# Optimization experiments

Measured on AMD Instinct MI355X. Metric: run time of the kernel, lower is better.

## Reference

```python
import jax, jax.numpy as jnp
import numpy as np

# Regularized layout for the per-batch masked attention:
#   batch_size B=8, each batch has NF=2048 'fill' points followed by NK=4096 'keep' points.
B, NF, NK = 8, 2048, 4096
C_IN, C_KQ, C_OUT = 256, 64, 256


def setup_inputs() -> dict:
    key = jax.random.key(0)
    ks = jax.random.split(key, 7)
    N = B * (NF + NK)
    features = jax.random.normal(ks[0], (N, C_IN), dtype=jnp.float32)
    # keep flag: 0 for fill points, 1 for keep points, per batch (fill-first layout)
    flag = jnp.tile(jnp.concatenate([jnp.zeros(NF, jnp.int32), jnp.ones(NK, jnp.int32)]), B)
    s = 1.0 / np.sqrt(C_IN)
    Wq = jax.random.normal(ks[1], (C_KQ, C_IN), jnp.float32) * s
    bq = jnp.zeros((C_KQ,), jnp.float32)
    Wk = jax.random.normal(ks[2], (C_KQ, C_IN), jnp.float32) * s
    bk = jnp.zeros((C_KQ,), jnp.float32)
    Wv = jax.random.normal(ks[3], (C_OUT, C_IN), jnp.float32) * s
    bv = jnp.zeros((C_OUT,), jnp.float32)
    return {"features": features, "keep_flag": flag,
            "Wq": Wq, "bq": bq, "Wk": Wk, "bk": bk, "Wv": Wv, "bv": bv}


def reference(features, keep_flag, Wq, bq, Wk, bk, Wv, bv):
    # features: [N, C_IN]; keep_flag encodes the fill/keep split, which in this
    # regular layout is: first NF rows of each batch are fill, remaining NK are keep.
    del keep_flag  # structure is encoded in the layout (fill-first per batch)
    f = features.reshape(B, NF + NK, C_IN)
    fill = f[:, :NF]             # [B, NF, C_IN]
    keep = f[:, NF:]             # [B, NK, C_IN]
    q = fill @ Wq.T + bq         # [B, NF, C_KQ]
    k = keep @ Wk.T + bk         # [B, NK, C_KQ]
    v = keep @ Wv.T + bv         # [B, NK, C_OUT]
    ratio = np.sqrt(C_KQ).astype(np.float32)
    scores = jnp.einsum('bfd,bkd->bfk', q, k) / ratio   # [B, NF, NK]
    attn = jax.nn.softmax(scores, axis=-1)
    out_fill = jnp.einsum('bfk,bkc->bfc', attn, v)      # [B, NF, C_OUT]
    # keep rows pass through unchanged (only fill rows are overwritten)
    out = jnp.concatenate([out_fill, keep], axis=1)
    return out.reshape(B * (NF + NK), C_OUT)
```

## Files before the change

kernel.cpp:

```cpp
#include <hip/hip_runtime.h>
#include <hip/hip_bf16.h>

#define BATCHES 8
#define NFILL 2048
#define NKEEP 4096
#define SEQLEN 6144
#define CIN 256
#define CKQ 64
#define COUT 256

#define KSC 0.18033688011112042f
#define KOFF -11.541560327111707f

typedef __bf16 bf16_t;
typedef float f32x4 __attribute__((ext_vector_type(4)));
typedef bf16_t bf16x8 __attribute__((ext_vector_type(8)));

__device__ inline void cvt8_store(bf16_t* dst, float4 a, float4 b) {
  bf16x8 v;
  v[0] = (bf16_t)a.x; v[1] = (bf16_t)a.y; v[2] = (bf16_t)a.z; v[3] = (bf16_t)a.w;
  v[4] = (bf16_t)b.x; v[5] = (bf16_t)b.y; v[6] = (bf16_t)b.z; v[7] = (bf16_t)b.w;
  *(bf16x8*)dst = v;
}

__device__ inline void proj_tile(const bf16_t (*Xs)[264], bf16_t (*Ws)[72],
                                 const float* __restrict__ Wmat, int lr,
                                 int koff, int wv, int l16, int quad,
                                 f32x4 acc[4]) {
  const float* wp = Wmat + (long)lr * CIN + koff;
  float4 w0 = *(const float4*)(wp);
  float4 w1 = *(const float4*)(wp + 4);
  float4 w2 = *(const float4*)(wp + 8);
  float4 w3 = *(const float4*)(wp + 12);
#pragma unroll
  for (int nb = 0; nb < 4; nb++) acc[nb] = f32x4{0.f, 0.f, 0.f, 0.f};
#pragma unroll
  for (int k0 = 0; k0 < CIN; k0 += 64) {
    const int kn = (k0 + 64 < CIN) ? k0 + 64 : k0;
    float4 n0 = *(const float4*)(wp + kn);
    float4 n1 = *(const float4*)(wp + kn + 4);
    float4 n2 = *(const float4*)(wp + kn + 8);
    float4 n3 = *(const float4*)(wp + kn + 12);
    __syncthreads();
    cvt8_store(&Ws[lr][koff], w0, w1);
    cvt8_store(&Ws[lr][koff + 8], w2, w3);
    __syncthreads();
#pragma unroll
    for (int ks = 0; ks < 2; ks++) {
      bf16x8 afrag = *(const bf16x8*)&Xs[wv * 16 + l16][k0 + ks * 32 + quad * 8];
#pragma unroll
      for (int nb = 0; nb < 4; nb++) {
        bf16x8 bfrag = *(const bf16x8*)&Ws[nb * 16 + l16][ks * 32 + quad * 8];
        acc[nb] = __builtin_amdgcn_mfma_f32_16x16x32_bf16(afrag, bfrag, acc[nb], 0, 0, 0);
      }
    }
    w0 = n0; w1 = n1; w2 = n2; w3 = n3;
  }
}

__global__ __launch_bounds__(256) void gemm_qkv(
    const float* __restrict__ feat, const float* __restrict__ Wq,
    const float* __restrict__ bq, const float* __restrict__ Wk,
    const float* __restrict__ bk, const float* __restrict__ Wv,
    const float* __restrict__ bv, bf16_t* __restrict__ Qw,
    bf16_t* __restrict__ Kw, bf16_t* __restrict__ Vw,
    float* __restrict__ outp) {
  __shared__ bf16_t Xs[64][264];
  __shared__ bf16_t Ws[64][72];
  __shared__ float Cs[64][68];

  const int bid = blockIdx.x;
  const bool isQ = bid >= 512;
  const int mb = isQ ? bid - 512 : bid;

  const int t = threadIdx.x;
  const int lane = t & 63;
  const int wv = t >> 6;
  const int l16 = lane & 15;
  const int quad = lane >> 4;

  const int lr = t >> 2;
  const int koff = (t & 3) << 4;

  const int mrow = mb * 64 + lr;
  const int rpb_shift = isQ ? 11 : 12;
  const int batch = mrow >> rpb_shift;
  const int ridx = mrow & ((1 << rpb_shift) - 1);
  const int row_off = isQ ? 0 : NFILL;
  const long grow = (long)(batch * SEQLEN + row_off + ridx);
  const float* xptr = feat + grow * CIN;
  float4* orow = (float4*)(outp + grow * COUT);

#pragma unroll
  for (int j = 0; j < 4; j++) {
    const int c = koff + j * 64;
    float4 x0 = *(const float4*)(xptr + c);
    float4 x1 = *(const float4*)(xptr + c + 4);
    float4 x2 = *(const float4*)(xptr + c + 8);
    float4 x3 = *(const float4*)(xptr + c + 12);
    cvt8_store(&Xs[lr][c], x0, x1);
    cvt8_store(&Xs[lr][c + 8], x2, x3);
    if (!isQ) {
      orow[(c >> 2) + 0] = x0;
      orow[(c >> 2) + 1] = x1;
      orow[(c >> 2) + 2] = x2;
      orow[(c >> 2) + 3] = x3;
    }
  }
  __syncthreads();

  f32x4 acc[4];

  if (isQ) {
    proj_tile(Xs, Ws, Wq, lr, koff, wv, l16, quad, acc);
#pragma unroll
    for (int nb = 0; nb < 4; nb++) {
      const int n = nb * 16 + l16;
      const float bb = bq[n];
#pragma unroll
      for (int r = 0; r < 4; r++) {
        const int m = mb * 64 + wv * 16 + quad * 4 + r;
        Qw[(long)m * CKQ + n] = (bf16_t)(acc[nb][r] + bb);
      }
    }
    return;
  }

  proj_tile(Xs, Ws, Wk, lr, koff, wv, l16, quad, acc);
#pragma unroll
  for (int nb = 0; nb < 4; nb++) {
    const int n = nb * 16 + l16;
    const float bb = bk[n];
#pragma unroll
    for (int r = 0; r < 4; r++) {
      const int m = mb * 64 + wv * 16 + quad * 4 + r;
      Kw[(long)m * CKQ + n] = (bf16_t)(acc[nb][r] + bb);
    }
  }

  const int vb = (mb * 64) >> 12;
  const int key0base = (mb * 64) & 4095;
  for (int nt = 0; nt < 4; nt++) {
    const int n0 = nt * 64;
    proj_tile(Xs, Ws, Wv + (long)n0 * CIN, lr, koff, wv, l16, quad, acc);

    __syncthreads();
#pragma unroll
    for (int nb = 0; nb < 4; nb++) {
      const float bb = bv[n0 + nb * 16 + l16];
#pragma unroll
      for (int r = 0; r < 4; r++)
        Cs[wv * 16 + quad * 4 + r][nb * 16 + l16] = acc[nb][r] + bb;
    }
    __syncthreads();
    const int c = t >> 2;
    const int seg = t & 3;
    bf16_t tmp[16];
#pragma unroll
    for (int i = 0; i < 16; i++) tmp[i] = (bf16_t)Cs[seg * 16 + i][c];
    bf16_t* dst = Vw + ((long)(vb * COUT + n0 + c)) * NKEEP + key0base + seg * 16;
    *(uint4*)dst = *(uint4*)tmp;
    *(uint4*)(dst + 8) = *(uint4*)(tmp + 8);
  }
}

__global__ __launch_bounds__(256) void attn_kernel(
    const bf16_t* __restrict__ Q, const bf16_t* __restrict__ K,
    const bf16_t* __restrict__ Vt, float* __restrict__ outp) {
  __shared__ bf16_t Ks[2][64][72];
  __shared__ bf16_t Ps[64][72];
  __shared__ float Lsh[64];

  const int qt = blockIdx.x;
  const int b = blockIdx.y;
  const int t = threadIdx.x;
  const int lane = t & 63;
  const int wv = t >> 6;
  const int l16 = lane & 15;
  const int quad = lane >> 4;

  const int krow = t >> 2;
  const int kcol = (t & 3) << 4;

  const bf16_t* kbase = K + (long)b * NKEEP * CKQ;
  const int c0 = wv * 64;
  const bf16_t* vlane =
      Vt + ((long)(b * COUT + c0 + l16)) * NKEEP + quad * 8;

  bf16x8 qfrag[2];
  {
    const bf16_t* qrow = Q + ((long)(b * NFILL + qt * 64 + wv * 16 + l16)) * CKQ;
#pragma unroll
    for (int ks = 0; ks < 2; ks++)
      qfrag[ks] = *(const bf16x8*)(qrow + ks * 32 + quad * 8);
  }

  f32x4 oacc[4][4];
#pragma unroll
  for (int m = 0; m < 4; m++)
#pragma unroll
    for (int ct = 0; ct < 4; ct++) oacc[m][ct] = f32x4{0.f, 0.f, 0.f, 0.f};
  float rsum[4] = {0.f, 0.f, 0.f, 0.f};

  uint4 kreg0, kreg1;
  bf16x8 vA[8], vB[8];

  {
    const bf16_t* ksrc = kbase + (long)krow * CKQ + kcol;
    uint4 k0 = *(const uint4*)ksrc;
    uint4 k1 = *(const uint4*)(ksrc + 8);
#pragma unroll
    for (int ct = 0; ct < 4; ct++)
#pragma unroll
      for (int ks = 0; ks < 2; ks++)
        vA[ct * 2 + ks] = *(const bf16x8*)(vlane + (long)ct * 16 * NKEEP + ks * 32);
    *(uint4*)&Ks[0][krow][kcol] = k0;
    *(uint4*)&Ks[0][krow][kcol + 8] = k1;
  }

#define ATTN_TILE(BUF, VCUR, VNEXT, TV)                                         \
  {                                                                             \
    __syncthreads(); \
    const int tn = ((TV) + 1 < 64) ? (TV) + 1 : 63;                             \
    {                                                                           \
      const bf16_t* ksrc = kbase + ((long)(tn * 64 + krow)) * CKQ + kcol;       \
      kreg0 = *(const uint4*)ksrc;                                              \
      kreg1 = *(const uint4*)(ksrc + 8);                                        \
      const bf16_t* vsrc = vlane + (long)tn * 64;                               \
      _Pragma("unroll") for (int ct = 0; ct < 4; ct++)                          \
          _Pragma("unroll") for (int ks = 0; ks < 2; ks++)                      \
              VNEXT[ct * 2 + ks] =                                              \
          *(const bf16x8*)(vsrc + (long)ct * 16 * NKEEP + ks * 32);             \
    }                                                                           \
    f32x4 sacc[4];                                                              \
    _Pragma("unroll") for (int nb = 0; nb < 4; nb++)                            \
        sacc[nb] = f32x4{0.f, 0.f, 0.f, 0.f};                                   \
    _Pragma("unroll") for (int ks = 0; ks < 2; ks++) {                          \
      _Pragma("unroll") for (int nb = 0; nb < 4; nb++) {                        \
        bf16x8 kfrag = *(const bf16x8*)&Ks[BUF][nb * 16 + l16][ks * 32 + quad * 8]; \
        sacc[nb] = __builtin_amdgcn_mfma_f32_16x16x32_bf16(qfrag[ks], kfrag,    \
                                                           sacc[nb], 0, 0, 0); \
      }                                                                         \
    }                                                                           \
    _Pragma("unroll") for (int nb = 0; nb < 4; nb++) {                          \
      _Pragma("unroll") for (int r = 0; r < 4; r++) {                           \
        const float p = __builtin_exp2f(fmaf(sacc[nb][r], KSC, KOFF));          \
        rsum[r] += p;                                                           \
        Ps[wv * 16 + quad * 4 + r][nb * 16 + l16] = (bf16_t)p;                  \
      }                                                                         \
    }                                                                           \
    asm volatile("s_waitcnt lgkmcnt(0)\n\ts_barrier" ::: "memory");      \
    _Pragma("unroll") for (int ks = 0; ks < 2; ks++) {                          \
      _Pragma("unroll") for (int m = 0; m < 4; m++) {                           \
        bf16x8 pfrag = *(const bf16x8*)&Ps[m * 16 + l16][ks * 32 + quad * 8];   \
        _Pragma("unroll") for (int ct = 0; ct < 4; ct++)                        \
            oacc[m][ct] = __builtin_amdgcn_mfma_f32_16x16x32_bf16(              \
                pfrag, VCUR[ct * 2 + ks], oacc[m][ct], 0, 0, 0);                \
      }                                                                         \
    }                                                                           \
    *(uint4*)&Ks[BUF ^ 1][krow][kcol] = kreg0;                                  \
    *(uint4*)&Ks[BUF ^ 1][krow][kcol + 8] = kreg1;                              \
  }

#pragma unroll 1
  for (int tv = 0; tv < 64; tv += 2) {
    ATTN_TILE(0, vA, vB, tv)
    ATTN_TILE(1, vB, vA, tv + 1)
  }
#undef ATTN_TILE

#pragma unroll
  for (int off = 1; off < 16; off <<= 1)
#pragma unroll
    for (int r = 0; r < 4; r++) rsum[r] += __shfl_xor(rsum[r], off, 64);
  if (l16 == 0) {
#pragma unroll
    for (int r = 0; r < 4; r++) Lsh[wv * 16 + quad * 4 + r] = rsum[r];
  }
  __syncthreads();

  float rl[4][4];
#pragma unroll
  for (int m = 0; m < 4; m++)
#pragma unroll
    for (int r = 0; r < 4; r++) rl[m][r] = 1.0f / Lsh[m * 16 + quad * 4 + r];

  const long obase = ((long)(b * SEQLEN + qt * 64)) * COUT + c0;
#pragma unroll
  for (int m = 0; m < 4; m++)
#pragma unroll
    for (int ct = 0; ct < 4; ct++)
#pragma unroll
      for (int r = 0; r < 4; r++)
        outp[obase + (long)(m * 16 + quad * 4 + r) * COUT + ct * 16 + l16] =
            oacc[m][ct][r] * rl[m][r];
}

extern "C" void kernel_launch(void* const* d_in, const int* in_sizes, int n_in,
                              void* d_out, int out_size, void* d_ws, size_t ws_size,
                              hipStream_t stream) {
  const float* feat = (const float*)d_in[0];
  const float* Wq = (const float*)d_in[2];
  const float* bq = (const float*)d_in[3];
  const float* Wk = (const float*)d_in[4];
  const float* bk = (const float*)d_in[5];
  const float* Wv = (const float*)d_in[6];
  const float* bv = (const float*)d_in[7];
  float* outp = (float*)d_out;

  bf16_t* Qw = (bf16_t*)d_ws;
  bf16_t* Kw = Qw + (size_t)BATCHES * NFILL * CKQ;
  bf16_t* Vw = Kw + (size_t)BATCHES * NKEEP * CKQ;

  gemm_qkv<<<dim3(768), 256, 0, stream>>>(feat, Wq, bq, Wk, bk, Wv, bv,
                                          Qw, Kw, Vw, outp);
  attn_kernel<<<dim3(NFILL / 64, BATCHES), 256, 0, stream>>>(Qw, Kw, Vw, outp);
}
```

Before: 207.1 us.

## Restructure QKV projection: full-K weight tile in LDS, register prefetch, swapped MFMA V output

The projection kernel now stages the whole 64x256 weight tile in shared memory at once, and prefetches the next weight tile into registers while the current one is used. This replaces the per-64-K chunk loop and its two barriers per chunk. For V, the MFMA operands are swapped so results come out already transposed and are stored directly, which removes the Cs shared-memory staging buffer and its extra barriers. It adds launch_bounds occupancy hint 2 and raw s_barrier asm, at the cost of more registers (64 floats of prefetch) and larger LDS use. The V stores become 2-byte scattered writes instead of 16-byte vectors.

```diff
diff --git a/kernel.cpp b/kernel.cpp
--- a/kernel.cpp
+++ b/kernel.cpp
@@ -23,42 +23,7 @@
   *(bf16x8*)dst = v;
 }
 
-__device__ inline void proj_tile(const bf16_t (*Xs)[264], bf16_t (*Ws)[72],
-                                 const float* __restrict__ Wmat, int lr,
-                                 int koff, int wv, int l16, int quad,
-                                 f32x4 acc[4]) {
-  const float* wp = Wmat + (long)lr * CIN + koff;
-  float4 w0 = *(const float4*)(wp);
-  float4 w1 = *(const float4*)(wp + 4);
-  float4 w2 = *(const float4*)(wp + 8);
-  float4 w3 = *(const float4*)(wp + 12);
-#pragma unroll
-  for (int nb = 0; nb < 4; nb++) acc[nb] = f32x4{0.f, 0.f, 0.f, 0.f};
-#pragma unroll
-  for (int k0 = 0; k0 < CIN; k0 += 64) {
-    const int kn = (k0 + 64 < CIN) ? k0 + 64 : k0;
-    float4 n0 = *(const float4*)(wp + kn);
-    float4 n1 = *(const float4*)(wp + kn + 4);
-    float4 n2 = *(const float4*)(wp + kn + 8);
-    float4 n3 = *(const float4*)(wp + kn + 12);
-    __syncthreads();
-    cvt8_store(&Ws[lr][koff], w0, w1);
-    cvt8_store(&Ws[lr][koff + 8], w2, w3);
-    __syncthreads();
-#pragma unroll
-    for (int ks = 0; ks < 2; ks++) {
-      bf16x8 afrag = *(const bf16x8*)&Xs[wv * 16 + l16][k0 + ks * 32 + quad * 8];
-#pragma unroll
-      for (int nb = 0; nb < 4; nb++) {
-        bf16x8 bfrag = *(const bf16x8*)&Ws[nb * 16 + l16][ks * 32 + quad * 8];
-        acc[nb] = __builtin_amdgcn_mfma_f32_16x16x32_bf16(afrag, bfrag, acc[nb], 0, 0, 0);
-      }
-    }
-    w0 = n0; w1 = n1; w2 = n2; w3 = n3;
-  }
-}
-
-__global__ __launch_bounds__(256) void gemm_qkv(
+__global__ __launch_bounds__(256, 2) void gemm_qkv(
     const float* __restrict__ feat, const float* __restrict__ Wq,
     const float* __restrict__ bq, const float* __restrict__ Wk,
     const float* __restrict__ bk, const float* __restrict__ Wv,
@@ -66,8 +31,7 @@
     bf16_t* __restrict__ Kw, bf16_t* __restrict__ Vw,
     float* __restrict__ outp) {
   __shared__ bf16_t Xs[64][264];
-  __shared__ bf16_t Ws[64][72];
-  __shared__ float Cs[64][68];
+  __shared__ bf16_t Ws[64][264];
 
   const int bid = blockIdx.x;
   const bool isQ = bid >= 512;
@@ -90,6 +54,16 @@
   const long grow = (long)(batch * SEQLEN + row_off + ridx);
   const float* xptr = feat + grow * CIN;
   float4* orow = (float4*)(outp + grow * COUT);
+
+  float4 wr[4][4];
+  {
+    const float* wrow0 = (isQ ? Wq : Wk) + (long)lr * CIN + koff;
+#pragma unroll
+    for (int j = 0; j < 4; j++)
+#pragma unroll
+      for (int s = 0; s < 4; s++)
+        wr[j][s] = *(const float4*)(wrow0 + j * 64 + s * 4);
+  }
 
 #pragma unroll
   for (int j = 0; j < 4; j++) {
@@ -109,58 +83,83 @@
   }
   __syncthreads();
 
-  f32x4 acc[4];
-
-  if (isQ) {
-    proj_tile(Xs, Ws, Wq, lr, koff, wv, l16, quad, acc);
-#pragma unroll
-    for (int nb = 0; nb < 4; nb++) {
-      const int n = nb * 16 + l16;
-      const float bb = bq[n];
-#pragma unroll
-      for (int r = 0; r < 4; r++) {
-        const int m = mb * 64 + wv * 16 + quad * 4 + r;
-        Qw[(long)m * CKQ + n] = (bf16_t)(acc[nb][r] + bb);
+  const int NT = isQ ? 1 : 5;
+  const int vb = (mb * 64) >> 12;
+  const int key0base = (mb * 64) & 4095;
+
+  for (int nt = 0; nt < NT; nt++) {
+#pragma unroll
+    for (int j = 0; j < 4; j++) {
+      cvt8_store(&Ws[lr][j * 64 + koff], wr[j][0], wr[j][1]);
+      cvt8_store(&Ws[lr][j * 64 + koff + 8], wr[j][2], wr[j][3]);
+    }
+    if (nt + 1 < NT) {
+      const float* wrow = Wv + ((long)(nt * 64) + lr) * CIN + koff;
+#pragma unroll
+      for (int j = 0; j < 4; j++)
+#pragma unroll
+        for (int s = 0; s < 4; s++)
+          wr[j][s] = *(const float4*)(wrow + j * 64 + s * 4);
+    }
+    asm volatile("s_waitcnt lgkmcnt(0)\n\ts_barrier" ::: "memory");
+
+    f32x4 acc[4];
+#pragma unroll
+    for (int nb = 0; nb < 4; nb++) acc[nb] = f32x4{0.f, 0.f, 0.f, 0.f};
+
+    if (nt == 0) {
+#pragma unroll
+      for (int k0 = 0; k0 < CIN; k0 += 64) {
+#pragma unroll
+        for (int ks = 0; ks < 2; ks++) {
+          bf16x8 afrag = *(const bf16x8*)&Xs[wv * 16 + l16][k0 + ks * 32 + quad * 8];
+#pragma unroll
+          for (int nb = 0; nb < 4; nb++) {
+            bf16x8 bfrag = *(const bf16x8*)&Ws[nb * 16 + l16][k0 + ks * 32 + quad * 8];
+            acc[nb] = __builtin_amdgcn_mfma_f32_16x16x32_bf16(afrag, bfrag, acc[nb], 0, 0, 0);
+          }
+        }
+      }
+      const float* bias = isQ ? bq : bk;
+      bf16_t* op = isQ ? Qw : Kw;
+#pragma unroll
+      for (int nb = 0; nb < 4; nb++) {
+        const int n = nb * 16 + l16;
+        const float bb = bias[n];
+#pragma unroll
+        for (int r = 0; r < 4; r++) {
+          const int m = mb * 64 + wv * 16 + quad * 4 + r;
+          op[(long)m * CKQ + n] = (bf16_t)(acc[nb][r] + bb);
+        }
+      }
+    } else {
+#pragma unroll
+      for (int k0 = 0; k0 < CIN; k0 += 64) {
+#pragma unroll
+        for (int ks = 0; ks < 2; ks++) {
+          bf16x8 xfrag = *(const bf16x8*)&Xs[wv * 16 + l16][k0 + ks * 32 + quad * 8];
+#pragma unroll
+          for (int nb = 0; nb < 4; nb++) {
+            bf16x8 wfrag = *(const bf16x8*)&Ws[nb * 16 + l16][k0 + ks * 32 + quad * 8];
+            acc[nb] = __builtin_amdgcn_mfma_f32_16x16x32_bf16(wfrag, xfrag, acc[nb], 0, 0, 0);
+          }
+        }
+      }
+      const int n0 = (nt - 1) * 64;
+#pragma unroll
+      for (int nb = 0; nb < 4; nb++) {
+        f32x4 bbv = *(const f32x4*)&bv[n0 + nb * 16 + quad * 4];
+        bf16_t* vdst = Vw +
+                       ((long)(vb * COUT + n0 + nb * 16 + quad * 4)) * NKEEP +
+                       key0base + wv * 16 + l16;
+#pragma unroll
+        for (int r = 0; r < 4; r++)
+          vdst[(long)r * NKEEP] = (bf16_t)(acc[nb][r] + bbv[r]);
       }
     }
-    return;
-  }
-
-  proj_tile(Xs, Ws, Wk, lr, koff, wv, l16, quad, acc);
-#pragma unroll
-  for (int nb = 0; nb < 4; nb++) {
-    const int n = nb * 16 + l16;
-    const float bb = bk[n];
-#pragma unroll
-    for (int r = 0; r < 4; r++) {
-      const int m = mb * 64 + wv * 16 + quad * 4 + r;
-      Kw[(long)m * CKQ + n] = (bf16_t)(acc[nb][r] + bb);
-    }
-  }
-
-  const int vb = (mb * 64) >> 12;
-  const int key0base = (mb * 64) & 4095;
-  for (int nt = 0; nt < 4; nt++) {
-    const int n0 = nt * 64;
-    proj_tile(Xs, Ws, Wv + (long)n0 * CIN, lr, koff, wv, l16, quad, acc);
-
-    __syncthreads();
-#pragma unroll
-    for (int nb = 0; nb < 4; nb++) {
-      const float bb = bv[n0 + nb * 16 + l16];
-#pragma unroll
-      for (int r = 0; r < 4; r++)
-        Cs[wv * 16 + quad * 4 + r][nb * 16 + l16] = acc[nb][r] + bb;
-    }
-    __syncthreads();
-    const int c = t >> 2;
-    const int seg = t & 3;
-    bf16_t tmp[16];
-#pragma unroll
-    for (int i = 0; i < 16; i++) tmp[i] = (bf16_t)Cs[seg * 16 + i][c];
-    bf16_t* dst = Vw + ((long)(vb * COUT + n0 + c)) * NKEEP + key0base + seg * 16;
-    *(uint4*)dst = *(uint4*)tmp;
-    *(uint4*)(dst + 8) = *(uint4*)(tmp + 8);
+
+    if (nt + 1 < NT)
+      asm volatile("s_waitcnt lgkmcnt(0)\n\ts_barrier" ::: "memory");
   }
 }
 
```

After: 204.3 us. No clear change (-1.4%).
